# Performance work log

Hardware: AMD Instinct MI355X
Metric: run time of the kernel (lower is better)

The kernel has to match this reference:

```python
import jax, jax.numpy as jnp
import numpy as np

N, E, F_IN, F_OUT = 50000, 800000, 256, 64


def setup_inputs() -> dict:
    key = jax.random.key(0)
    k1, k2, k3, k4 = jax.random.split(key, 4)
    x = jax.random.normal(k1, (N, F_IN), dtype=jnp.float32)
    adj = jax.random.randint(k2, (2, E), 0, N, dtype=jnp.int32)
    # GCNConv parameters (glorot-ish init)
    W = jax.random.normal(k3, (F_IN, F_OUT), dtype=jnp.float32) / np.sqrt(F_IN)
    b = jnp.zeros((F_OUT,), dtype=jnp.float32)
    return {"x": x, "adj": adj, "W": W, "b": b}


def reference(x, adj, W, b):
    n = x.shape[0]
    # PyG GCNConv: add self-loops, symmetric normalization D^-1/2 A D^-1/2
    loop = jnp.arange(n, dtype=adj.dtype)
    src = jnp.concatenate([adj[0], loop])  # [E+N]
    dst = jnp.concatenate([adj[1], loop])  # [E+N]
    deg = jax.ops.segment_sum(jnp.ones_like(dst, dtype=x.dtype), dst, num_segments=n)
    dinv = jax.lax.rsqrt(deg)  # deg >= 1 due to self-loops
    norm = dinv[src] * dinv[dst]  # [E+N]
    h = x @ W  # [N, F_OUT] — transform before propagate (GCNConv order)
    msg = h[src] * norm[:, None]  # [E+N, F_OUT]
    out = jax.ops.segment_sum(msg, dst, num_segments=n) + b
    return jax.nn.relu(out)
```

## Files before the change

kernel.cpp:

```cpp
#include <hip/hip_runtime.h>

#define F_IN 256
#define F_OUT 64
#define BSH 7
#define BINW 128
#define NBINS_CAP 512
#define BATCH 4096
#define CSTRIDE 16
#define MAXBIN_CAP 2560

typedef __attribute__((ext_vector_type(8))) short short8;
typedef __attribute__((ext_vector_type(4))) float f32x4;

__device__ inline float bf_lo(unsigned u) { return __uint_as_float(u << 16); }
__device__ inline float bf_hi(unsigned u) { return __uint_as_float(u & 0xFFFF0000u); }
__device__ inline unsigned cvt_pk_bf16(float lo, float hi) {
    unsigned r;
    asm("v_cvt_pk_bf16_f32 %0, %1, %2" : "=v"(r) : "v"(lo), "v"(hi));
    return r;
}
__device__ inline short8 pack_cvt(float4 a, float4 b) {
    union { unsigned u[4]; short8 s; } r;
    r.u[0] = cvt_pk_bf16(a.x, a.y);
    r.u[1] = cvt_pk_bf16(a.z, a.w);
    r.u[2] = cvt_pk_bf16(b.x, b.y);
    r.u[3] = cvt_pk_bf16(b.z, b.w);
    return r.s;
}

__global__ __launch_bounds__(256) void bin_count(const int* __restrict__ adj,
                                                 unsigned* __restrict__ staging,
                                                 int* __restrict__ cursor,
                                                 int E, int nbins, int maxBin) {
    __shared__ int cnt[NBINS_CAP];
    __shared__ int base[NBINS_CAP];
    const int tid = threadIdx.x;
    for (int i = tid; i < NBINS_CAP; i += 256) cnt[i] = 0;
    __syncthreads();

    const int e0 = blockIdx.x * BATCH + tid * 16;
    int S[16], D[16], sl[16];
    int nv = 0;
    if (e0 + 16 <= E) {
#pragma unroll
        for (int k = 0; k < 4; k++) {
            *(int4*)&S[k * 4] = *(const int4*)&adj[e0 + k * 4];
            *(int4*)&D[k * 4] = *(const int4*)&adj[E + e0 + k * 4];
        }
        nv = 16;
    } else if (e0 < E) {
        for (int k = 0; k < 16 && e0 + k < E; k++) {
            S[k] = adj[e0 + k];
            D[k] = adj[E + e0 + k];
            nv++;
        }
    }
#pragma unroll
    for (int j = 0; j < 16; j++) {
        if (j < nv) sl[j] = atomicAdd(&cnt[D[j] >> BSH], 1);
    }
    __syncthreads();
    for (int i = tid; i < nbins; i += 256) {
        int cv = cnt[i];
        base[i] = cv ? atomicAdd(&cursor[i * CSTRIDE], cv) : 0;
    }
    __syncthreads();
#pragma unroll
    for (int j = 0; j < 16; j++) {
        if (j < nv) {
            int b = D[j] >> BSH;
            int pos = base[b] + sl[j];
            if (pos < maxBin)
                staging[(size_t)b * maxBin + pos] =
                    (unsigned)S[j] | ((unsigned)(D[j] & (BINW - 1)) << 16);
        }
    }
}

__global__ __launch_bounds__(512, 4) void gemm_mfma(const float* __restrict__ x,
                                                    const float* __restrict__ W,
                                                    const unsigned* __restrict__ staging,
                                                    const int* __restrict__ cursor,
                                                    unsigned* __restrict__ gu,
                                                    int N, int maxBin) {
    __shared__ unsigned Wf[32 * 64 * 4];
    __shared__ int degL[BINW];
    __shared__ float dinvL[BINW];
    const int b = blockIdx.x;
    const int tid = threadIdx.x;

    if (tid < BINW) degL[tid] = 0;
    for (int p = tid; p < (F_IN / 2) * F_OUT; p += 512) {
        int kp = p >> 6;
        int n = p & 63;
        int k = kp * 2;
        Wf[((k >> 3) * 64 + n) * 4 + ((k & 7) >> 1)] =
            cvt_pk_bf16(W[k * F_OUT + n], W[(k + 1) * F_OUT + n]);
    }
    __syncthreads();

    const int segCnt = min(cursor[b * CSTRIDE], maxBin);
    const unsigned* seg = staging + (size_t)b * maxBin;
    for (int i = tid; i < segCnt; i += 512) atomicAdd(&degL[seg[i] >> 16], 1);
    __syncthreads();
    if (tid < BINW) dinvL[tid] = rsqrtf((float)degL[tid] + 1.0f);
    __syncthreads();

    const int wave = tid >> 6;
    const int lane = tid & 63;
    const int q = lane >> 4;
    const int c = lane & 15;
    const int n0 = b * 128 + wave * 16;
    const int r = min(n0 + c, N - 1);
    const float* p0 = x + (size_t)r * F_IN + q * 8;

    f32x4 acc[4] = {};
#pragma unroll
    for (int s = 0; s < 8; s++) {
        float4 a0 = *(const float4*)(p0 + s * 32);
        float4 a1 = *(const float4*)(p0 + s * 32 + 4);
        short8 ah = pack_cvt(a0, a1);
#pragma unroll
        for (int t = 0; t < 4; t++) {
            short8 bh = *(const short8*)&Wf[((s * 4 + q) * 64 + t * 16 + c) * 4];
            acc[t] = __builtin_amdgcn_mfma_f32_16x16x32_bf16(ah, bh, acc[t], 0, 0, 0);
        }
    }

#pragma unroll
    for (int rr = 0; rr < 4; rr++) {
        int node = n0 + q * 4 + rr;
        float dv = dinvL[wave * 16 + q * 4 + rr];
#pragma unroll
        for (int t = 0; t < 4; t++) {
            float v = acc[t][rr] * dv;
            float o = __shfl_xor(v, 1, 64);
            if (node < N && !(lane & 1)) {
                gu[(size_t)node * 32 + t * 8 + (c >> 1)] = cvt_pk_bf16(v, o);
            }
        }
    }
}

__global__ __launch_bounds__(512) void gather_bin(const unsigned* __restrict__ staging,
                                                  const int* __restrict__ cursor,
                                                  const unsigned* __restrict__ g32,
                                                  const float* __restrict__ bias,
                                                  float* __restrict__ out,
                                                  int N, int maxBin) {
    __shared__ int cnt[BINW];
    __shared__ int off[BINW];
    __shared__ int wsum[2];
    __shared__ unsigned short binCsr[MAXBIN_CAP];
    const int b = blockIdx.x;
    const int tid = threadIdx.x;
    const int nb0 = b << BSH;

    if (tid < BINW) cnt[tid] = 0;
    __syncthreads();

    const int segCnt = min(cursor[b * CSTRIDE], maxBin);
    const unsigned* seg = staging + (size_t)b * maxBin;

    unsigned ev[5];
    int sl[5];
    int nv = 0;
#pragma unroll
    for (int r = 0; r < 5; r++) {
        int i = tid + r * 512;
        if (i < segCnt) {
            unsigned e = seg[i];
            ev[r] = e;
            sl[r] = atomicAdd(&cnt[e >> 16], 1);
            nv = r + 1;
        }
    }
    __syncthreads();

    int incl = 0, v = 0;
    if (tid < BINW) {
        v = cnt[tid];
        incl = v;
        const int lane = tid & 63;
        for (int d = 1; d < 64; d <<= 1) {
            int t = __shfl_up(incl, d, 64);
            if (lane >= d) incl += t;
        }
        if (lane == 63) wsum[tid >> 6] = incl;
    }
    __syncthreads();
    if (tid < BINW) off[tid] = incl - v + ((tid >= 64) ? wsum[0] : 0);
    __syncthreads();

#pragma unroll
    for (int r = 0; r < 5; r++) {
        if (r < nv) binCsr[off[ev[r] >> 16] + sl[r]] = (unsigned short)(ev[r] & 0xFFFFu);
    }
    __syncthreads();

    const int wv = tid >> 6;
    const int lane = tid & 63;
    const int grp = lane >> 3;
    const int h = lane & 7;
    const uint4* g4 = (const uint4*)g32;

    for (int t = 0; t < 16; t++) {
        const int node = wv * 16 + t;
        const int gn = nb0 + node;
        if (gn >= N) break;
        const int start = off[node];
        const int deg = cnt[node];

        float a0[8] = {}, a1[8] = {};
        int i = grp;
        for (; i + 8 < deg; i += 16) {
            int s0 = binCsr[start + i], s1 = binCsr[start + i + 8];
            uint4 u0 = g4[(size_t)s0 * 8 + h];
            uint4 u1 = g4[(size_t)s1 * 8 + h];
            a0[0] += bf_lo(u0.x); a0[1] += bf_hi(u0.x);
            a0[2] += bf_lo(u0.y); a0[3] += bf_hi(u0.y);
            a0[4] += bf_lo(u0.z); a0[5] += bf_hi(u0.z);
            a0[6] += bf_lo(u0.w); a0[7] += bf_hi(u0.w);
            a1[0] += bf_lo(u1.x); a1[1] += bf_hi(u1.x);
            a1[2] += bf_lo(u1.y); a1[3] += bf_hi(u1.y);
            a1[4] += bf_lo(u1.z); a1[5] += bf_hi(u1.z);
            a1[6] += bf_lo(u1.w); a1[7] += bf_hi(u1.w);
        }
        if (i < deg) {
            int s0 = binCsr[start + i];
            uint4 u0 = g4[(size_t)s0 * 8 + h];
            a0[0] += bf_lo(u0.x); a0[1] += bf_hi(u0.x);
            a0[2] += bf_lo(u0.y); a0[3] += bf_hi(u0.y);
            a0[4] += bf_lo(u0.z); a0[5] += bf_hi(u0.z);
            a0[6] += bf_lo(u0.w); a0[7] += bf_hi(u0.w);
        }
        float acc[8];
#pragma unroll
        for (int k = 0; k < 8; k++) acc[k] = a0[k] + a1[k];
#pragma unroll
        for (int m = 8; m < 64; m <<= 1) {
#pragma unroll
            for (int k = 0; k < 8; k++) acc[k] += __shfl_xor(acc[k], m, 64);
        }
        if (grp == 0) {
            uint4 us = g4[(size_t)gn * 8 + h];
            float dv = rsqrtf((float)deg + 1.0f);
            float s0 = bf_lo(us.x), s1 = bf_hi(us.x), s2 = bf_lo(us.y), s3 = bf_hi(us.y);
            float s4 = bf_lo(us.z), s5 = bf_hi(us.z), s6 = bf_lo(us.w), s7 = bf_hi(us.w);
            float4 b0 = *(const float4*)&bias[h * 8];
            float4 b1 = *(const float4*)&bias[h * 8 + 4];
            float4 r0, r1;
            r0.x = fmaxf(fmaf(dv, acc[0] + s0, b0.x), 0.0f);
            r0.y = fmaxf(fmaf(dv, acc[1] + s1, b0.y), 0.0f);
            r0.z = fmaxf(fmaf(dv, acc[2] + s2, b0.z), 0.0f);
            r0.w = fmaxf(fmaf(dv, acc[3] + s3, b0.w), 0.0f);
            r1.x = fmaxf(fmaf(dv, acc[4] + s4, b1.x), 0.0f);
            r1.y = fmaxf(fmaf(dv, acc[5] + s5, b1.y), 0.0f);
            r1.z = fmaxf(fmaf(dv, acc[6] + s6, b1.z), 0.0f);
            r1.w = fmaxf(fmaf(dv, acc[7] + s7, b1.w), 0.0f);
            *(float4*)&out[(size_t)gn * F_OUT + h * 8] = r0;
            *(float4*)&out[(size_t)gn * F_OUT + h * 8 + 4] = r1;
        }
    }
}

extern "C" void kernel_launch(void* const* d_in, const int* in_sizes, int n_in,
                              void* d_out, int out_size, void* d_ws, size_t ws_size,
                              hipStream_t stream) {
    const float* x = (const float*)d_in[0];
    const int* adj = (const int*)d_in[1];
    const float* W = (const float*)d_in[2];
    const float* b = (const float*)d_in[3];
    float* out = (float*)d_out;

    const int N = in_sizes[0] / F_IN;
    const int E = in_sizes[1] / 2;
    const int nbins = (N + BINW - 1) >> BSH;
    const int maxBin = MAXBIN_CAP;

    char* ws = (char*)d_ws;
    size_t segCur = (((size_t)nbins * CSTRIDE * 4) + 255) & ~(size_t)255;
    size_t segStg = (((size_t)nbins * maxBin * 4) + 255) & ~(size_t)255;
    int* cursor = (int*)ws;
    unsigned* staging = (unsigned*)(ws + segCur);
    unsigned* g16 = (unsigned*)(ws + segCur + segStg);

    hipMemsetAsync(cursor, 0, segCur, stream);

    bin_count<<<(E + BATCH - 1) / BATCH, 256, 0, stream>>>(adj, staging, cursor,
                                                           E, nbins, maxBin);
    gemm_mfma<<<nbins, 512, 0, stream>>>(x, W, staging, cursor, g16, N, maxBin);
    gather_bin<<<nbins, 512, 0, stream>>>(staging, cursor, g16, b, out, N, maxBin);
}
```

Baseline: 149.5 us.

## Compute node degrees with global atomics in binning pass, shrink GEMM blocks

The binning kernel now also increments a global per-node degree array with an atomic per edge. The GEMM kernel no longer scans its bin's staging segment to build degrees. It reads degrees directly and processes 64 nodes per 256-thread block, which doubles the block count and improves load spread. The cost is 800K extra global atomics in the binning pass, in exchange for removing the serialized shared-memory degree scan and two barriers from the GEMM.

```diff
diff --git a/kernel.cpp b/kernel.cpp
--- a/kernel.cpp
+++ b/kernel.cpp
@@ -28,10 +28,11 @@
     return r.s;
 }
 
-__global__ __launch_bounds__(256) void bin_count(const int* __restrict__ adj,
-                                                 unsigned* __restrict__ staging,
-                                                 int* __restrict__ cursor,
-                                                 int E, int nbins, int maxBin) {
+__global__ __launch_bounds__(256) void bin_deg(const int* __restrict__ adj,
+                                               unsigned* __restrict__ staging,
+                                               int* __restrict__ cursor,
+                                               int* __restrict__ deg,
+                                               int E, int nbins, int maxBin) {
     __shared__ int cnt[NBINS_CAP];
     __shared__ int base[NBINS_CAP];
     const int tid = threadIdx.x;
@@ -57,7 +58,10 @@
     }
 #pragma unroll
     for (int j = 0; j < 16; j++) {
-        if (j < nv) sl[j] = atomicAdd(&cnt[D[j] >> BSH], 1);
+        if (j < nv) {
+            sl[j] = atomicAdd(&cnt[D[j] >> BSH], 1);
+            atomicAdd(&deg[D[j]], 1);
+        }
     }
     __syncthreads();
     for (int i = tid; i < nbins; i += 256) {
@@ -77,20 +81,21 @@
     }
 }
 
-__global__ __launch_bounds__(512, 4) void gemm_mfma(const float* __restrict__ x,
+__global__ __launch_bounds__(256, 4) void gemm_mfma(const float* __restrict__ x,
                                                     const float* __restrict__ W,
-                                                    const unsigned* __restrict__ staging,
-                                                    const int* __restrict__ cursor,
-                                                    unsigned* __restrict__ gu,
-                                                    int N, int maxBin) {
+                                                    const int* __restrict__ deg,
+                                                    unsigned* __restrict__ gu, int N) {
     __shared__ unsigned Wf[32 * 64 * 4];
-    __shared__ int degL[BINW];
-    __shared__ float dinvL[BINW];
+    __shared__ float dinvL[64];
     const int b = blockIdx.x;
     const int tid = threadIdx.x;
-
-    if (tid < BINW) degL[tid] = 0;
-    for (int p = tid; p < (F_IN / 2) * F_OUT; p += 512) {
+    const int nb0 = b * 64;
+
+    if (tid < 64) {
+        int gn = min(nb0 + tid, N - 1);
+        dinvL[tid] = rsqrtf((float)deg[gn] + 1.0f);
+    }
+    for (int p = tid; p < (F_IN / 2) * F_OUT; p += 256) {
         int kp = p >> 6;
         int n = p & 63;
         int k = kp * 2;
@@ -99,18 +104,11 @@
     }
     __syncthreads();
 
-    const int segCnt = min(cursor[b * CSTRIDE], maxBin);
-    const unsigned* seg = staging + (size_t)b * maxBin;
-    for (int i = tid; i < segCnt; i += 512) atomicAdd(&degL[seg[i] >> 16], 1);
-    __syncthreads();
-    if (tid < BINW) dinvL[tid] = rsqrtf((float)degL[tid] + 1.0f);
-    __syncthreads();
-
     const int wave = tid >> 6;
     const int lane = tid & 63;
     const int q = lane >> 4;
     const int c = lane & 15;
-    const int n0 = b * 128 + wave * 16;
+    const int n0 = nb0 + wave * 16;
     const int r = min(n0 + c, N - 1);
     const float* p0 = x + (size_t)r * F_IN + q * 8;
 
@@ -277,18 +275,21 @@
     const int E = in_sizes[1] / 2;
     const int nbins = (N + BINW - 1) >> BSH;
     const int maxBin = MAXBIN_CAP;
+    const int nhalf = (N + 63) / 64;
 
     char* ws = (char*)d_ws;
     size_t segCur = (((size_t)nbins * CSTRIDE * 4) + 255) & ~(size_t)255;
+    size_t segDeg = (((size_t)N * 4) + 255) & ~(size_t)255;
     size_t segStg = (((size_t)nbins * maxBin * 4) + 255) & ~(size_t)255;
     int* cursor = (int*)ws;
-    unsigned* staging = (unsigned*)(ws + segCur);
-    unsigned* g16 = (unsigned*)(ws + segCur + segStg);
-
-    hipMemsetAsync(cursor, 0, segCur, stream);
-
-    bin_count<<<(E + BATCH - 1) / BATCH, 256, 0, stream>>>(adj, staging, cursor,
-                                                           E, nbins, maxBin);
-    gemm_mfma<<<nbins, 512, 0, stream>>>(x, W, staging, cursor, g16, N, maxBin);
+    int* deg = (int*)(ws + segCur);
+    unsigned* staging = (unsigned*)(ws + segCur + segDeg);
+    unsigned* g16 = (unsigned*)(ws + segCur + segDeg + segStg);
+
+    hipMemsetAsync(cursor, 0, segCur + segDeg, stream);
+
+    bin_deg<<<(E + BATCH - 1) / BATCH, 256, 0, stream>>>(adj, staging, cursor,
+                                                         deg, E, nbins, maxBin);
+    gemm_mfma<<<nhalf, 256, 0, stream>>>(x, W, deg, g16, N);
     gather_bin<<<nbins, 512, 0, stream>>>(staging, cursor, g16, b, out, N, maxBin);
 }
```

New measurement: 180.4 us. 1.21x slower.
